# Performance work log

Hardware: AMD Instinct MI355X
Metric: run time of the kernel (lower is better)

The kernel has to match this reference:

```python
import jax, jax.numpy as jnp
import numpy as np

D_MODEL = 768
NUM_HEADS = 12
D_K = D_MODEL // NUM_HEADS
B, T = 2, 4096


def setup_inputs() -> dict:
    key = jax.random.key(0)
    ks = jax.random.split(key, 5)
    x = jax.random.normal(ks[0], (B, T, D_MODEL), dtype=jnp.float32)
    # causal mask: True = masked (matches masked_fill semantics)
    mask = jnp.triu(jnp.ones((T, T), dtype=bool), k=1)
    W_qkv = jax.random.normal(ks[1], (D_MODEL, 3 * D_MODEL), dtype=jnp.float32) / np.sqrt(D_MODEL)
    b_qkv = jax.random.normal(ks[2], (3 * D_MODEL,), dtype=jnp.float32) * 0.02
    W_out = jax.random.normal(ks[3], (D_MODEL, D_MODEL), dtype=jnp.float32) / np.sqrt(D_MODEL)
    b_out = jax.random.normal(ks[4], (D_MODEL,), dtype=jnp.float32) * 0.02
    return {"x": x, "mask": mask, "W_qkv": W_qkv, "b_qkv": b_qkv, "W_out": W_out, "b_out": b_out}


def reference(x, mask, W_qkv, b_qkv, W_out, b_out):
    Bb, Tt, C = x.shape
    qkv = x @ W_qkv + b_qkv                       # [B,T,3C]
    # torch: reshape(B,T,H,3*d_k).transpose(1,2) then chunk on last dim
    qkv = qkv.reshape(Bb, Tt, NUM_HEADS, 3, D_K)  # split each head's 3*d_k chunk
    qkv = jnp.transpose(qkv, (0, 2, 1, 3, 4))     # [B,H,T,3,d_k]
    q, k, v = qkv[..., 0, :], qkv[..., 1, :], qkv[..., 2, :]
    scores = jnp.einsum('bhqd,bhkd->bhqk', q, k) / np.sqrt(D_K)
    scores = jnp.where(mask[None, None], -jnp.inf, scores)
    attn = jax.nn.softmax(scores, axis=-1)
    context = jnp.einsum('bhqk,bhkd->bhqd', attn, v)
    context = jnp.transpose(context, (0, 2, 1, 3)).reshape(Bb, Tt, C)
    return context @ W_out + b_out
```

## Files before the change

### kernel.cpp

```cpp
#include <hip/hip_runtime.h>
#include <hip/hip_bf16.h>
#include <stdint.h>


typedef __attribute__((ext_vector_type(8))) short bf16x8;
typedef __attribute__((ext_vector_type(4))) short bf16x4;
typedef __attribute__((ext_vector_type(4))) float f32x4;

#define TT 4096
#define NH 12
#define DK 64
#define DMODEL 768
#define NQKV 2304

__device__ __forceinline__ unsigned short f2bf(float f) {
    union { float f; unsigned u; } v; v.f = f;
    unsigned u = v.u;
    return (unsigned short)((u + 0x7fffu + ((u >> 16) & 1u)) >> 16);
}
__device__ __forceinline__ unsigned fbits(float f) {
    union { float f; unsigned u; } v; v.f = f; return v.u;
}
__device__ __forceinline__ unsigned pack_bf2(float a, float b) {
    return __builtin_amdgcn_perm(fbits(b) + 0x8000u, fbits(a) + 0x8000u, 0x07060302u);
}
__device__ __forceinline__ void glds16(const void* g, void* l) {
    __builtin_amdgcn_global_load_lds(
        (const __attribute__((address_space(1))) void*)g,
        (__attribute__((address_space(3))) void*)l, 16, 0, 0);
}

__global__ __launch_bounds__(256) void xbf_kernel(const float* __restrict__ x,
                                                  unsigned short* __restrict__ xb) {
    int i = (blockIdx.x * 256 + threadIdx.x) * 4;
    float4 v = *(const float4*)(x + i);
    uint2 u;
    u.x = (unsigned)f2bf(v.x) | ((unsigned)f2bf(v.y) << 16);
    u.y = (unsigned)f2bf(v.z) | ((unsigned)f2bf(v.w) << 16);
    *(uint2*)(xb + i) = u;
}

__global__ __launch_bounds__(256) void wt_kernel(const float* __restrict__ W,
                                                 unsigned short* __restrict__ Wt,
                                                 int K, int N) {
    __shared__ unsigned short tile[64][65];
    int k0 = blockIdx.y * 64, n0 = blockIdx.x * 64;
    int c = threadIdx.x & 63;
    int r0 = threadIdx.x >> 6;
    for (int p = 0; p < 16; ++p) {
        int r = r0 + p * 4;
        tile[r][c] = f2bf(W[(size_t)(k0 + r) * N + n0 + c]);
    }
    __syncthreads();
    for (int p = 0; p < 16; ++p) {
        int n = r0 + p * 4;
        Wt[(size_t)(n0 + n) * K + k0 + c] = tile[c][n];
    }
}

__global__ __launch_bounds__(256, 2)
void gemm_qkv(const unsigned short* __restrict__ Amat, const unsigned short* __restrict__ Bmat,
              const float* __restrict__ bias, unsigned short* __restrict__ qb,
              unsigned short* __restrict__ kb, unsigned short* __restrict__ vtb) {
    __shared__ unsigned short As[128 * 64];
    __shared__ unsigned short Bs[128 * 64];
    const int K = DMODEL;
    int m0 = blockIdx.y * 128, n0 = blockIdx.x * 128;
    int tid = threadIdx.x, lane = tid & 63, w = tid >> 6;
    int wm = (w >> 1) * 64, wn = (w & 1) * 64;
    int quad = lane >> 4, lc = lane & 15;

    const unsigned short* agp[4]; const unsigned short* bgp[4];
    unsigned short* alp[4]; unsigned short* blp[4];
    for (int p = 0; p < 4; ++p) {
        int c = (w * 4 + p) * 64 + lane;
        int row = c >> 3, pc = c & 7;
        int gc = pc ^ (row & 7);
        agp[p] = Amat + (size_t)(m0 + row) * K + gc * 8;
        bgp[p] = Bmat + (size_t)(n0 + row) * K + gc * 8;
        alp[p] = &As[(w * 4 + p) * 512];
        blp[p] = &Bs[(w * 4 + p) * 512];
    }
    int foff[4][2];
    for (int mt = 0; mt < 4; ++mt)
        for (int h = 0; h < 2; ++h)
            foff[mt][h] = (mt * 16 + lc) * 64 + (((quad + 4 * h) ^ (lc & 7)) * 8);

    f32x4 acc[4][4];
    for (int a = 0; a < 4; ++a)
        for (int b2 = 0; b2 < 4; ++b2) acc[a][b2] = (f32x4){0.f, 0.f, 0.f, 0.f};

    for (int k0 = 0; k0 < K; k0 += 64) {
        for (int p = 0; p < 4; ++p) {
            glds16(agp[p] + k0, alp[p]);
            glds16(bgp[p] + k0, blp[p]);
        }
        __syncthreads();
        bf16x8 af[4][2], bfr[4][2];
        for (int mt = 0; mt < 4; ++mt)
            for (int h = 0; h < 2; ++h) {
                af[mt][h]  = *(const bf16x8*)(&As[wm * 64 + foff[mt][h]]);
                bfr[mt][h] = *(const bf16x8*)(&Bs[wn * 64 + foff[mt][h]]);
            }
        for (int mt = 0; mt < 4; ++mt)
            for (int nt = 0; nt < 4; ++nt) {
                acc[mt][nt] = __builtin_amdgcn_mfma_f32_16x16x32_bf16(
                    af[mt][0], bfr[nt][0], acc[mt][nt], 0, 0, 0);
                acc[mt][nt] = __builtin_amdgcn_mfma_f32_16x16x32_bf16(
                    af[mt][1], bfr[nt][1], acc[mt][nt], 0, 0, 0);
            }
        __syncthreads();
    }
    const float c2q = 0.18033688f;
    for (int mt = 0; mt < 4; ++mt) {
        int colv = m0 + wm + mt * 16 + quad * 4;
        float4 bv = *(const float4*)(bias + colv);
        int h = colv / 192;
        int r = colv - h * 192;
        int which = r >> 6;
        int d0 = r & 63;
        for (int nt = 0; nt < 4; ++nt) {
            int tok = n0 + wn + nt * 16 + lc;
            int b = tok >> 12, t = tok & 4095;
            size_t bh = (size_t)(b * NH + h);
            float v0 = acc[mt][nt][0] + bv.x, v1 = acc[mt][nt][1] + bv.y;
            float v2 = acc[mt][nt][2] + bv.z, v3 = acc[mt][nt][3] + bv.w;
            if (which == 0) {
                uint2 u;
                u.x = pack_bf2(v0 * c2q, v1 * c2q);
                u.y = pack_bf2(v2 * c2q, v3 * c2q);
                *(uint2*)(qb + (bh * TT + t) * DK + d0) = u;
            } else if (which == 1) {
                uint2 u;
                u.x = pack_bf2(v0, v1);
                u.y = pack_bf2(v2, v3);
                *(uint2*)(kb + (bh * TT + t) * DK + d0) = u;
            } else {
                unsigned short* vp = vtb + (bh * DK + d0) * TT + t;
                vp[0] = f2bf(v0); vp[TT] = f2bf(v1);
                vp[2 * TT] = f2bf(v2); vp[3 * TT] = f2bf(v3);
            }
        }
    }
}

__global__ __launch_bounds__(256)
void flash_attn(const unsigned short* __restrict__ qbuf,
                const unsigned short* __restrict__ kbuf,
                const unsigned short* __restrict__ vtbuf,
                unsigned short* __restrict__ ctx) {
    __shared__ unsigned short Ks[2][64 * 64];
    __shared__ unsigned short Vs[2][64 * 64];
    int bh = blockIdx.x;
    int qblk = 63 - (int)blockIdx.y;
    int tid = threadIdx.x, lane = tid & 63, w = tid >> 6;
    int quad = lane >> 4, lc = lane & 15;
    const size_t base = (size_t)bh * TT * DK;
    const unsigned short* kb = kbuf + base;
    const unsigned short* vb = vtbuf + base;
    int col8 = ((lane & 7) ^ (lane >> 3)) * 8;
    int klane = (lane >> 3) * DK + col8;
    int vlane = (lane >> 3) * TT + col8;
    size_t hb = (size_t)(bh / NH) * TT * DMODEL + (size_t)(bh % NH) * DK;

    int q_lo = qblk * 64 + w * 16;
    int ntile = qblk + 1;

    bf16x8 qf0, qf1;
    {
        const unsigned short* qp = qbuf + base + (size_t)(q_lo + lc) * DK;
        qf0 = *(const bf16x8*)(qp + quad * 8);
        qf1 = *(const bf16x8*)(qp + 32 + quad * 8);
    }
    f32x4 o[4];
    for (int dt = 0; dt < 4; ++dt) o[dt] = (f32x4){0.f, 0.f, 0.f, 0.f};
    float lsum = 0.f;

    {
        int rb = (w & 1) * 4;
        if (w < 2)
            for (int r = 0; r < 4; ++r)
                glds16(kb + (size_t)((rb + r) * 8) * DK + klane, &Ks[0][(rb + r) * 512]);
        else
            for (int r = 0; r < 4; ++r)
                glds16(vb + (size_t)((rb + r) * 8) * TT + vlane, &Vs[0][(rb + r) * 512]);
    }
    __syncthreads();

    for (int ti = 0; ti < ntile; ++ti) {
        int cur = ti & 1;
        if (ti + 1 < ntile) {
            int kn = (ti + 1) * 64;
            int rb = (w & 1) * 4;
            if (w < 2)
                for (int r = 0; r < 4; ++r)
                    glds16(kb + (size_t)(kn + (rb + r) * 8) * DK + klane,
                           &Ks[cur ^ 1][(rb + r) * 512]);
            else
                for (int r = 0; r < 4; ++r)
                    glds16(vb + (size_t)((rb + r) * 8) * TT + kn + vlane,
                           &Vs[cur ^ 1][(rb + r) * 512]);
        }
        int kt = ti * 64;
        const unsigned short* Kb = &Ks[cur][0];
        const unsigned short* Vb = &Vs[cur][0];
        bool diag = (ti == ntile - 1);
        uint2 pp[4];
        int c0 = quad ^ (lc & 7);
        for (int ktile = 0; ktile < 4; ++ktile) {
            bf16x8 kf0 = *(const bf16x8*)(&Kb[(ktile * 16 + lc) * 64 + c0 * 8]);
            bf16x8 kf1 = *(const bf16x8*)(&Kb[(ktile * 16 + lc) * 64 + (c0 ^ 4) * 8]);
            f32x4 s = (f32x4){0.f, 0.f, 0.f, 0.f};
            s = __builtin_amdgcn_mfma_f32_16x16x32_bf16(kf0, qf0, s, 0, 0, 0);
            s = __builtin_amdgcn_mfma_f32_16x16x32_bf16(kf1, qf1, s, 0, 0, 0);
            int key0 = kt + ktile * 16 + quad * 4;
            int qcol = q_lo + lc;
            float p[4];
            for (int i = 0; i < 4; ++i) {
                float e = __builtin_amdgcn_exp2f(s[i]);
                if (diag && (key0 + i > qcol)) e = 0.f;
                p[i] = e;
            }
            lsum += (p[0] + p[1]) + (p[2] + p[3]);
            pp[ktile].x = pack_bf2(p[0], p[1]);
            pp[ktile].y = pack_bf2(p[2], p[3]);
        }
        for (int dt = 0; dt < 4; ++dt) {
            int row = dt * 16 + lc;
            int sw = lc & 7;
            for (int ktile = 0; ktile < 4; ++ktile) {
                int c8 = (ktile * 2 + (quad >> 1)) ^ sw;
                bf16x4 vf = *(const bf16x4*)(&Vb[row * 64 + c8 * 8 + (quad & 1) * 4]);
                union { uint2 u; bf16x4 v; } pc; pc.u = pp[ktile];
                o[dt] = __builtin_amdgcn_mfma_f32_16x16x16bf16_1k(
                    vf, pc.v, o[dt], 0, 0, 0);
            }
        }
        __syncthreads();
    }

    float l = lsum;
    l += __shfl_xor(l, 16, 64);
    l += __shfl_xor(l, 32, 64);
    float inv = 1.f / l;
    int t = q_lo + lc;
    unsigned short* cp = ctx + hb + (size_t)t * DMODEL;
    for (int dt = 0; dt < 4; ++dt) {
        uint2 u;
        u.x = pack_bf2(o[dt][0] * inv, o[dt][1] * inv);
        u.y = pack_bf2(o[dt][2] * inv, o[dt][3] * inv);
        *(uint2*)(cp + dt * 16 + quad * 4) = u;
    }
}

__global__ __launch_bounds__(256, 2)
void gemm_out(const unsigned short* __restrict__ Amat, const unsigned short* __restrict__ Bmat,
              const float* __restrict__ bias, float* __restrict__ out) {
    __shared__ unsigned short As[128 * 64];
    __shared__ unsigned short Bs[128 * 64];
    const int K = DMODEL;
    int m0 = blockIdx.y * 128, n0 = blockIdx.x * 128;
    int tid = threadIdx.x, lane = tid & 63, w = tid >> 6;
    int wm = (w >> 1) * 64, wn = (w & 1) * 64;
    int quad = lane >> 4, lc = lane & 15;

    const unsigned short* agp[4]; const unsigned short* bgp[4];
    unsigned short* alp[4]; unsigned short* blp[4];
    for (int p = 0; p < 4; ++p) {
        int c = (w * 4 + p) * 64 + lane;
        int row = c >> 3, pc = c & 7;
        int gc = pc ^ (row & 7);
        agp[p] = Amat + (size_t)(m0 + row) * K + gc * 8;
        bgp[p] = Bmat + (size_t)(n0 + row) * K + gc * 8;
        alp[p] = &As[(w * 4 + p) * 512];
        blp[p] = &Bs[(w * 4 + p) * 512];
    }
    int foff[4][2];
    for (int mt = 0; mt < 4; ++mt)
        for (int h = 0; h < 2; ++h)
            foff[mt][h] = (mt * 16 + lc) * 64 + (((quad + 4 * h) ^ (lc & 7)) * 8);

    f32x4 acc[4][4];
    for (int a = 0; a < 4; ++a)
        for (int b2 = 0; b2 < 4; ++b2) acc[a][b2] = (f32x4){0.f, 0.f, 0.f, 0.f};

    for (int k0 = 0; k0 < K; k0 += 64) {
        for (int p = 0; p < 4; ++p) {
            glds16(agp[p] + k0, alp[p]);
            glds16(bgp[p] + k0, blp[p]);
        }
        __syncthreads();
        bf16x8 af[4][2], bfr[4][2];
        for (int mt = 0; mt < 4; ++mt)
            for (int h = 0; h < 2; ++h) {
                af[mt][h]  = *(const bf16x8*)(&As[wm * 64 + foff[mt][h]]);
                bfr[mt][h] = *(const bf16x8*)(&Bs[wn * 64 + foff[mt][h]]);
            }
        for (int mt = 0; mt < 4; ++mt)
            for (int nt = 0; nt < 4; ++nt) {
                acc[mt][nt] = __builtin_amdgcn_mfma_f32_16x16x32_bf16(
                    af[mt][0], bfr[nt][0], acc[mt][nt], 0, 0, 0);
                acc[mt][nt] = __builtin_amdgcn_mfma_f32_16x16x32_bf16(
                    af[mt][1], bfr[nt][1], acc[mt][nt], 0, 0, 0);
            }
        __syncthreads();
    }
    for (int mt = 0; mt < 4; ++mt) {
        int colv = m0 + wm + mt * 16 + quad * 4;
        float4 bv = *(const float4*)(bias + colv);
        for (int nt = 0; nt < 4; ++nt) {
            int tok = n0 + wn + nt * 16 + lc;
            float4 ov;
            ov.x = acc[mt][nt][0] + bv.x;
            ov.y = acc[mt][nt][1] + bv.y;
            ov.z = acc[mt][nt][2] + bv.z;
            ov.w = acc[mt][nt][3] + bv.w;
            *(float4*)(out + (size_t)tok * DMODEL + colv) = ov;
        }
    }
}

extern "C" void kernel_launch(void* const* d_in, const int* in_sizes, int n_in,
                              void* d_out, int out_size, void* d_ws, size_t ws_size,
                              hipStream_t stream) {
    const float* x     = (const float*)d_in[0];
    const float* W_qkv = (const float*)d_in[2];
    const float* b_qkv = (const float*)d_in[3];
    const float* W_out = (const float*)d_in[4];
    const float* b_out = (const float*)d_in[5];
    float* out = (float*)d_out;

    unsigned short* ws = (unsigned short*)d_ws;
    unsigned short* Wqkv_t = ws;
    unsigned short* Wout_t = Wqkv_t + (size_t)NQKV * DMODEL;
    unsigned short* q_buf  = Wout_t + (size_t)DMODEL * DMODEL;
    unsigned short* k_buf  = q_buf  + (size_t)2 * NH * TT * DK;
    unsigned short* vt_buf = k_buf  + (size_t)2 * NH * TT * DK;
    unsigned short* ctx    = vt_buf + (size_t)2 * NH * TT * DK;
    unsigned short* x_bf   = ctx;

    xbf_kernel<<<dim3((2 * TT * DMODEL) / (256 * 4)), 256, 0, stream>>>(x, x_bf);
    wt_kernel<<<dim3(NQKV / 64, DMODEL / 64), 256, 0, stream>>>(W_qkv, Wqkv_t, DMODEL, NQKV);
    wt_kernel<<<dim3(DMODEL / 64, DMODEL / 64), 256, 0, stream>>>(W_out, Wout_t, DMODEL, DMODEL);
    gemm_qkv<<<dim3((2 * TT) / 128, NQKV / 128), 256, 0, stream>>>(
        Wqkv_t, x_bf, b_qkv, q_buf, k_buf, vt_buf);
    flash_attn<<<dim3(2 * NH, TT / 64), 256, 0, stream>>>(q_buf, k_buf, vt_buf, ctx);
    gemm_out<<<dim3((2 * TT) / 128, DMODEL / 128), 256, 0, stream>>>(
        Wout_t, ctx, b_out, out);
}
```

Before: 271.3 us.

## Merge prep kernels, specialize diagonal attention tile, retile output GEMM

Three prep launches (x conversion and two weight transposes) are merged into one kernel that dispatches on block index. The flash attention inner tile is templated on whether it is the diagonal tile, so non-diagonal tiles skip the mask compare, and the PV MFMAs are interleaved per key subtile instead of a separate loop. The output GEMM moves from 128x128 to 64x128 tiles to launch twice as many blocks across the CUs. Each block then carries less reuse per loaded byte, and the launch-bounds occupancy hint is removed.

```diff
diff --git a/kernel.cpp b/kernel.cpp
--- a/kernel.cpp
+++ b/kernel.cpp
@@ -30,21 +30,30 @@
         (__attribute__((address_space(3))) void*)l, 16, 0, 0);
 }
 
-__global__ __launch_bounds__(256) void xbf_kernel(const float* __restrict__ x,
-                                                  unsigned short* __restrict__ xb) {
-    int i = (blockIdx.x * 256 + threadIdx.x) * 4;
-    float4 v = *(const float4*)(x + i);
-    uint2 u;
-    u.x = (unsigned)f2bf(v.x) | ((unsigned)f2bf(v.y) << 16);
-    u.y = (unsigned)f2bf(v.z) | ((unsigned)f2bf(v.w) << 16);
-    *(uint2*)(xb + i) = u;
-}
-
-__global__ __launch_bounds__(256) void wt_kernel(const float* __restrict__ W,
-                                                 unsigned short* __restrict__ Wt,
-                                                 int K, int N) {
+__global__ __launch_bounds__(256)
+void prep(const float* __restrict__ x, unsigned short* __restrict__ xb,
+          const float* __restrict__ Wq, unsigned short* __restrict__ Wqt,
+          const float* __restrict__ Wo, unsigned short* __restrict__ Wot) {
+    int b = blockIdx.x;
+    if (b < 6144) {
+        int i = (b * 256 + threadIdx.x) * 4;
+        float4 v = *(const float4*)(x + i);
+        uint2 u;
+        u.x = pack_bf2(v.x, v.y);
+        u.y = pack_bf2(v.z, v.w);
+        *(uint2*)(xb + i) = u;
+        return;
+    }
     __shared__ unsigned short tile[64][65];
-    int k0 = blockIdx.y * 64, n0 = blockIdx.x * 64;
+    const float* W; unsigned short* Wt; int K, N, bx, by;
+    if (b < 6144 + 432) {
+        int bb = b - 6144; bx = bb % 36; by = bb / 36;
+        W = Wq; Wt = Wqt; K = DMODEL; N = NQKV;
+    } else {
+        int bb = b - 6576; bx = bb % 12; by = bb / 12;
+        W = Wo; Wt = Wot; K = DMODEL; N = DMODEL;
+    }
+    int k0 = by * 64, n0 = bx * 64;
     int c = threadIdx.x & 63;
     int r0 = threadIdx.x >> 6;
     for (int p = 0; p < 16; ++p) {
@@ -144,6 +153,45 @@
     }
 }
 
+template <bool DIAG>
+__device__ __forceinline__ void flash_tile(const unsigned short* __restrict__ Kb,
+                                           const unsigned short* __restrict__ Vb,
+                                           bf16x8 qf0, bf16x8 qf1,
+                                           f32x4 (&o)[4], float& lsum,
+                                           int kt, int q_lo, int quad, int lc) {
+    int c0 = quad ^ (lc & 7);
+    int sw = lc & 7;
+    for (int ktile = 0; ktile < 4; ++ktile) {
+        bf16x8 kf0 = *(const bf16x8*)(&Kb[(ktile * 16 + lc) * 64 + c0 * 8]);
+        bf16x8 kf1 = *(const bf16x8*)(&Kb[(ktile * 16 + lc) * 64 + (c0 ^ 4) * 8]);
+        f32x4 s = (f32x4){0.f, 0.f, 0.f, 0.f};
+        s = __builtin_amdgcn_mfma_f32_16x16x32_bf16(kf0, qf0, s, 0, 0, 0);
+        s = __builtin_amdgcn_mfma_f32_16x16x32_bf16(kf1, qf1, s, 0, 0, 0);
+        float p[4];
+        if (DIAG) {
+            int key0 = kt + ktile * 16 + quad * 4;
+            int qcol = q_lo + lc;
+            for (int i = 0; i < 4; ++i) {
+                float e = __builtin_amdgcn_exp2f(s[i]);
+                if (key0 + i > qcol) e = 0.f;
+                p[i] = e;
+            }
+        } else {
+            for (int i = 0; i < 4; ++i) p[i] = __builtin_amdgcn_exp2f(s[i]);
+        }
+        lsum += (p[0] + p[1]) + (p[2] + p[3]);
+        union { uint2 u; bf16x4 v; } pc;
+        pc.u.x = pack_bf2(p[0], p[1]);
+        pc.u.y = pack_bf2(p[2], p[3]);
+        int c8 = (ktile * 2 + (quad >> 1)) ^ sw;
+        int voff = c8 * 8 + (quad & 1) * 4;
+        for (int dt = 0; dt < 4; ++dt) {
+            bf16x4 vf = *(const bf16x4*)(&Vb[(dt * 16 + lc) * 64 + voff]);
+            o[dt] = __builtin_amdgcn_mfma_f32_16x16x16bf16_1k(vf, pc.v, o[dt], 0, 0, 0);
+        }
+    }
+}
+
 __global__ __launch_bounds__(256)
 void flash_attn(const unsigned short* __restrict__ qbuf,
                 const unsigned short* __restrict__ kbuf,
@@ -202,40 +250,12 @@
                            &Vs[cur ^ 1][(rb + r) * 512]);
         }
         int kt = ti * 64;
-        const unsigned short* Kb = &Ks[cur][0];
-        const unsigned short* Vb = &Vs[cur][0];
-        bool diag = (ti == ntile - 1);
-        uint2 pp[4];
-        int c0 = quad ^ (lc & 7);
-        for (int ktile = 0; ktile < 4; ++ktile) {
-            bf16x8 kf0 = *(const bf16x8*)(&Kb[(ktile * 16 + lc) * 64 + c0 * 8]);
-            bf16x8 kf1 = *(const bf16x8*)(&Kb[(ktile * 16 + lc) * 64 + (c0 ^ 4) * 8]);
-            f32x4 s = (f32x4){0.f, 0.f, 0.f, 0.f};
-            s = __builtin_amdgcn_mfma_f32_16x16x32_bf16(kf0, qf0, s, 0, 0, 0);
-            s = __builtin_amdgcn_mfma_f32_16x16x32_bf16(kf1, qf1, s, 0, 0, 0);
-            int key0 = kt + ktile * 16 + quad * 4;
-            int qcol = q_lo + lc;
-            float p[4];
-            for (int i = 0; i < 4; ++i) {
-                float e = __builtin_amdgcn_exp2f(s[i]);
-                if (diag && (key0 + i > qcol)) e = 0.f;
-                p[i] = e;
-            }
-            lsum += (p[0] + p[1]) + (p[2] + p[3]);
-            pp[ktile].x = pack_bf2(p[0], p[1]);
-            pp[ktile].y = pack_bf2(p[2], p[3]);
-        }
-        for (int dt = 0; dt < 4; ++dt) {
-            int row = dt * 16 + lc;
-            int sw = lc & 7;
-            for (int ktile = 0; ktile < 4; ++ktile) {
-                int c8 = (ktile * 2 + (quad >> 1)) ^ sw;
-                bf16x4 vf = *(const bf16x4*)(&Vb[row * 64 + c8 * 8 + (quad & 1) * 4]);
-                union { uint2 u; bf16x4 v; } pc; pc.u = pp[ktile];
-                o[dt] = __builtin_amdgcn_mfma_f32_16x16x16bf16_1k(
-                    vf, pc.v, o[dt], 0, 0, 0);
-            }
-        }
+        if (ti == ntile - 1)
+            flash_tile<true>(&Ks[cur][0], &Vs[cur][0], qf0, qf1, o, lsum,
+                             kt, q_lo, quad, lc);
+        else
+            flash_tile<false>(&Ks[cur][0], &Vs[cur][0], qf0, qf1, o, lsum,
+                              kt, q_lo, quad, lc);
         __syncthreads();
     }
 
@@ -253,50 +273,50 @@
     }
 }
 
-__global__ __launch_bounds__(256, 2)
+__global__ __launch_bounds__(256)
 void gemm_out(const unsigned short* __restrict__ Amat, const unsigned short* __restrict__ Bmat,
               const float* __restrict__ bias, float* __restrict__ out) {
-    __shared__ unsigned short As[128 * 64];
-    __shared__ unsigned short Bs[128 * 64];
+    __shared__ unsigned short S[(64 + 128) * 64];
     const int K = DMODEL;
-    int m0 = blockIdx.y * 128, n0 = blockIdx.x * 128;
+    int m0 = blockIdx.y * 64, n0 = blockIdx.x * 128;
     int tid = threadIdx.x, lane = tid & 63, w = tid >> 6;
-    int wm = (w >> 1) * 64, wn = (w & 1) * 64;
+    int wm = (w & 1) * 32, wn = (w >> 1) * 64;
     int quad = lane >> 4, lc = lane & 15;
 
-    const unsigned short* agp[4]; const unsigned short* bgp[4];
-    unsigned short* alp[4]; unsigned short* blp[4];
-    for (int p = 0; p < 4; ++p) {
-        int c = (w * 4 + p) * 64 + lane;
-        int row = c >> 3, pc = c & 7;
-        int gc = pc ^ (row & 7);
-        agp[p] = Amat + (size_t)(m0 + row) * K + gc * 8;
-        bgp[p] = Bmat + (size_t)(n0 + row) * K + gc * 8;
-        alp[p] = &As[(w * 4 + p) * 512];
-        blp[p] = &Bs[(w * 4 + p) * 512];
-    }
-    int foff[4][2];
-    for (int mt = 0; mt < 4; ++mt)
+    const unsigned short* gp[6]; unsigned short* lp[6];
+    for (int p = 0; p < 6; ++p) {
+        int c = (w * 6 + p) * 64 + lane;
+        if (c < 512) {
+            int row = c >> 3, gc = (c & 7) ^ (row & 7);
+            gp[p] = Amat + (size_t)(m0 + row) * K + gc * 8;
+        } else {
+            int cb = c - 512;
+            int row = cb >> 3, gc = (cb & 7) ^ (row & 7);
+            gp[p] = Bmat + (size_t)(n0 + row) * K + gc * 8;
+        }
+        lp[p] = &S[(w * 6 + p) * 512];
+    }
+    int foffA[2][2], foffB[4][2];
+    for (int mt = 0; mt < 2; ++mt)
         for (int h = 0; h < 2; ++h)
-            foff[mt][h] = (mt * 16 + lc) * 64 + (((quad + 4 * h) ^ (lc & 7)) * 8);
-
-    f32x4 acc[4][4];
-    for (int a = 0; a < 4; ++a)
+            foffA[mt][h] = (wm + mt * 16 + lc) * 64 + (((quad + 4 * h) ^ (lc & 7)) * 8);
+    for (int nt = 0; nt < 4; ++nt)
+        for (int h = 0; h < 2; ++h)
+            foffB[nt][h] = 4096 + (wn + nt * 16 + lc) * 64 + (((quad + 4 * h) ^ (lc & 7)) * 8);
+
+    f32x4 acc[2][4];
+    for (int a = 0; a < 2; ++a)
         for (int b2 = 0; b2 < 4; ++b2) acc[a][b2] = (f32x4){0.f, 0.f, 0.f, 0.f};
 
     for (int k0 = 0; k0 < K; k0 += 64) {
-        for (int p = 0; p < 4; ++p) {
-            glds16(agp[p] + k0, alp[p]);
-            glds16(bgp[p] + k0, blp[p]);
-        }
-        __syncthreads();
-        bf16x8 af[4][2], bfr[4][2];
-        for (int mt = 0; mt < 4; ++mt)
-            for (int h = 0; h < 2; ++h) {
-                af[mt][h]  = *(const bf16x8*)(&As[wm * 64 + foff[mt][h]]);
-                bfr[mt][h] = *(const bf16x8*)(&Bs[wn * 64 + foff[mt][h]]);
-            }
-        for (int mt = 0; mt < 4; ++mt)
+        for (int p = 0; p < 6; ++p) glds16(gp[p] + k0, lp[p]);
+        __syncthreads();
+        bf16x8 af[2][2], bfr[4][2];
+        for (int mt = 0; mt < 2; ++mt)
+            for (int h = 0; h < 2; ++h) af[mt][h] = *(const bf16x8*)(&S[foffA[mt][h]]);
+        for (int nt = 0; nt < 4; ++nt)
+            for (int h = 0; h < 2; ++h) bfr[nt][h] = *(const bf16x8*)(&S[foffB[nt][h]]);
+        for (int mt = 0; mt < 2; ++mt)
             for (int nt = 0; nt < 4; ++nt) {
                 acc[mt][nt] = __builtin_amdgcn_mfma_f32_16x16x32_bf16(
                     af[mt][0], bfr[nt][0], acc[mt][nt], 0, 0, 0);
@@ -305,7 +325,7 @@
             }
         __syncthreads();
     }
-    for (int mt = 0; mt < 4; ++mt) {
+    for (int mt = 0; mt < 2; ++mt) {
         int colv = m0 + wm + mt * 16 + quad * 4;
         float4 bv = *(const float4*)(bias + colv);
         for (int nt = 0; nt < 4; ++nt) {
@@ -339,12 +359,10 @@
     unsigned short* ctx    = vt_buf + (size_t)2 * NH * TT * DK;
     unsigned short* x_bf   = ctx;
 
-    xbf_kernel<<<dim3((2 * TT * DMODEL) / (256 * 4)), 256, 0, stream>>>(x, x_bf);
-    wt_kernel<<<dim3(NQKV / 64, DMODEL / 64), 256, 0, stream>>>(W_qkv, Wqkv_t, DMODEL, NQKV);
-    wt_kernel<<<dim3(DMODEL / 64, DMODEL / 64), 256, 0, stream>>>(W_out, Wout_t, DMODEL, DMODEL);
+    prep<<<dim3(6720), 256, 0, stream>>>(x, x_bf, W_qkv, Wqkv_t, W_out, Wout_t);
     gemm_qkv<<<dim3((2 * TT) / 128, NQKV / 128), 256, 0, stream>>>(
         Wqkv_t, x_bf, b_qkv, q_buf, k_buf, vt_buf);
     flash_attn<<<dim3(2 * NH, TT / 64), 256, 0, stream>>>(q_buf, k_buf, vt_buf, ctx);
-    gemm_out<<<dim3((2 * TT) / 128, DMODEL / 128), 256, 0, stream>>>(
+    gemm_out<<<dim3((2 * TT) / 128, DMODEL / 64), 256, 0, stream>>>(
         Wout_t, ctx, b_out, out);
 }
```

Measured after the change: 261.5 us. 3.6% less time.
